# Kernel tuning notes

Measured on AMD Instinct MI355X. Metric: run time of the kernel, lower is better.

## Reference

```python
import jax, jax.numpy as jnp
import numpy as np

B, N, DIM = 2, 1024, 512
HEADS, DIM_HEAD = 8, 64
HIDDEN = HEADS * DIM_HEAD
TIME_DIM = 512
BIAS_DIM = 16
EPS = 1e-5


def setup_inputs() -> dict:
    key = jax.random.key(0)
    ks = jax.random.split(key, 12)
    inp = {
        "x": jax.random.normal(ks[0], (B, N, DIM), jnp.float32),
        "residx": jnp.broadcast_to(jnp.arange(N, dtype=jnp.float32), (B, N)),
        "time": jax.random.normal(ks[1], (B, 1, TIME_DIM), jnp.float32),
        "attn_bias": jax.random.normal(ks[2], (B, BIAS_DIM, N, N), jnp.float32),
        "seq_mask": jnp.ones((B, N), jnp.float32),
        # params
        "gamma": jnp.ones((DIM,), jnp.float32),
        "Wt": jax.random.normal(ks[3], (2 * DIM, TIME_DIM), jnp.float32) * 0.02,
        "bt": jax.random.normal(ks[4], (2 * DIM,), jnp.float32) * 0.02,
        "Wb": jax.random.normal(ks[5], (HEADS, BIAS_DIM), jnp.float32) * 0.1,
        "bb": jax.random.normal(ks[6], (HEADS,), jnp.float32) * 0.1,
        "Wq": jax.random.normal(ks[7], (HIDDEN, DIM), jnp.float32) * (DIM ** -0.5),
        "Wkv": jax.random.normal(ks[8], (2 * HIDDEN, DIM), jnp.float32) * (DIM ** -0.5),
        "Wo": jax.random.normal(ks[9], (DIM, HIDDEN), jnp.float32) * (HIDDEN ** -0.5),
    }
    return inp


def _layer_norm(x, gamma):
    mu = jnp.mean(x, axis=-1, keepdims=True)
    var = jnp.var(x, axis=-1, keepdims=True)
    return (x - mu) * jax.lax.rsqrt(var + EPS) * gamma  # beta buffer is zeros


def reference(x, residx, time, attn_bias, seq_mask, gamma, Wt, bt, Wb, bb, Wq, Wkv, Wo):
    h, d = HEADS, DIM_HEAD
    b, n, _ = x.shape
    xn = _layer_norm(x, gamma)
    # time conditioning: SiLU -> Linear -> chunk into scale/shift
    t = jax.nn.silu(time) @ Wt.T + bt  # [B,1,2*dim]
    scale, shift = jnp.split(t, 2, axis=-1)
    xn = xn * (scale + 1.0) + shift
    xn = xn * seq_mask[..., None]
    # projections
    q = (xn @ Wq.T).reshape(b, n, h, d).transpose(0, 2, 1, 3)  # b h n d
    kv = xn @ Wkv.T
    k_, v_ = jnp.split(kv, 2, axis=-1)
    k = k_.reshape(b, n, h, d).transpose(0, 2, 1, 3)
    v = v_.reshape(b, n, h, d).transpose(0, 2, 1, 3)
    q = q * (d ** -0.5)
    sim = jnp.einsum('bhid,bhjd->bhij', q, k)
    # attn bias projection: b a i j -> linear over a -> b h i j
    bias = jnp.einsum('baij,ha->bhij', attn_bias, Wb) + bb[None, :, None, None]
    sim = sim + bias
    # mask
    attn_mask = seq_mask[:, None, :, None] * seq_mask[:, None, None, :]  # b 1 i j
    sim = sim - (1.0 - attn_mask) * 1e6
    attn = jax.nn.softmax(sim, axis=-1)
    out = jnp.einsum('bhij,bhjd->bhid', attn, v)
    out = out.transpose(0, 2, 1, 3).reshape(b, n, h * d)
    out = out @ Wo.T
    out = out * seq_mask[..., None]
    return out
```

## Files before the change

### kernel.cpp

```cpp
#include <hip/hip_runtime.h>
#include <cstdint>
#include <cstddef>

typedef __bf16 bf16x8 __attribute__((ext_vector_type(8)));
typedef float f32x4 __attribute__((ext_vector_type(4)));
typedef unsigned int u32x4 __attribute__((ext_vector_type(4)));
typedef unsigned short u16;
typedef unsigned short u16x8 __attribute__((ext_vector_type(8)));

__device__ __forceinline__ u16 f2b(float f) {
    union { float f; uint32_t u; } v; v.f = f;
    uint32_t r = v.u + 0x7fffu + ((v.u >> 16) & 1u);
    return (u16)(r >> 16);
}
__device__ __forceinline__ float b2f(u16 h) {
    union { uint32_t u; float f; } v; v.u = ((uint32_t)h) << 16; return v.f;
}

__global__ __launch_bounds__(256) void prep_kernel(
    const float* __restrict__ Wq, const float* __restrict__ Wkv, const float* __restrict__ Wo,
    const float* __restrict__ timep, const float* __restrict__ Wt, const float* __restrict__ bt,
    u16* __restrict__ wqkv, u16* __restrict__ wo, float* __restrict__ tbuf)
{
    __shared__ float st[512];
    int bx = blockIdx.x, tid = threadIdx.x;
    if (bx < 1024) {
        int i = bx * 256 + tid;
        float4 v; u16* dp;
        if (i < 65536)      { v = ((const float4*)Wq)[i];            dp = wqkv + (size_t)i * 4; }
        else if (i < 196608){ int k = i - 65536;  v = ((const float4*)Wkv)[k]; dp = wqkv + 262144 + (size_t)k * 4; }
        else                { int k = i - 196608; v = ((const float4*)Wo)[k];  dp = wo + (size_t)k * 4; }
        ushort4 o;
        o.x = f2b(v.x); o.y = f2b(v.y); o.z = f2b(v.z); o.w = f2b(v.w);
        *(ushort4*)dp = o;
    } else {
        int bx2 = bx - 1024;
        int b = bx2 >> 2, ch = bx2 & 3;
        for (int k = tid; k < 512; k += 256) {
            float v = timep[b * 512 + k];
            st[k] = v / (1.f + __expf(-v));
        }
        __syncthreads();
        int o = ch * 256 + tid;
        const float4* wrow = (const float4*)(Wt + (size_t)o * 512);
        float acc = bt[o];
        #pragma unroll 4
        for (int k4 = 0; k4 < 128; k4++) {
            float4 w = wrow[k4];
            acc += st[k4*4+0]*w.x + st[k4*4+1]*w.y + st[k4*4+2]*w.z + st[k4*4+3]*w.w;
        }
        tbuf[b * 1024 + o] = acc;
    }
}

__global__ __launch_bounds__(64) void ln_cond_kernel(
    const float* __restrict__ x, const float* __restrict__ gamma,
    const float* __restrict__ tbuf, const float* __restrict__ seq_mask,
    u16* __restrict__ xn)
{
    int m = blockIdx.x;
    int b = m >> 10;
    int lane = threadIdx.x;
    const float* xr = x + (size_t)m * 512;
    int c0 = lane * 8;
    float4 v0 = *(const float4*)(xr + c0);
    float4 v1 = *(const float4*)(xr + c0 + 4);
    float xv[8] = {v0.x, v0.y, v0.z, v0.w, v1.x, v1.y, v1.z, v1.w};
    float s = 0.f, ss = 0.f;
    #pragma unroll
    for (int e = 0; e < 8; e++) { s += xv[e]; ss += xv[e]*xv[e]; }
    #pragma unroll
    for (int off = 1; off < 64; off <<= 1) {
        s  += __shfl_xor(s, off);
        ss += __shfl_xor(ss, off);
    }
    float mu = s * (1.f/512.f);
    float var = ss * (1.f/512.f) - mu*mu;
    float rs = rsqrtf(var + 1e-5f);
    float mk = seq_mask[m];
    u16x8 ov;
    #pragma unroll
    for (int e = 0; e < 8; e++) {
        int c = c0 + e;
        float sc = tbuf[b*1024 + c] + 1.f;
        float sh = tbuf[b*1024 + 512 + c];
        float val = ((xv[e] - mu) * rs * gamma[c] * sc + sh) * mk;
        ov[e] = f2b(val);
    }
    *(u16x8*)&xn[(size_t)m * 512 + c0] = ov;
}

__global__ __launch_bounds__(256) void bias_kernel(
    const float* __restrict__ ab, const float* __restrict__ Wb, const float* __restrict__ bbv,
    u16* __restrict__ bias_t)
{
    __shared__ u16 Ts[8 * 16 * 68];
    __shared__ float wbs[128];
    __shared__ float bbs[8];
    const int tid = threadIdx.x, bx = blockIdx.x;
    if (tid < 128) wbs[tid] = Wb[tid];
    if (tid < 8) bbs[tid] = bbv[tid];
    __syncthreads();
    int b = bx >> 10;
    int rem = bx & 1023;
    int i16 = rem >> 4, jt = rem & 15;
    int il = tid >> 4, jq = tid & 15;
    int i = i16*16 + il, j = jt*64 + jq*4;
    const float* p = ab + ((size_t)b << 24) + ((size_t)i << 10) + j;

#define LD(n) f32x4 v##n = __builtin_nontemporal_load((const f32x4*)(p + ((size_t)(n) << 20)));
    LD(0) LD(1) LD(2) LD(3) LD(4) LD(5) LD(6) LD(7)
    LD(8) LD(9) LD(10) LD(11) LD(12) LD(13) LD(14) LD(15)
#undef LD
#define FMAS(h) \
    f32x4 a##h = {bbs[h], bbs[h], bbs[h], bbs[h]}; \
    a##h += wbs[(h)*16+ 0]*v0;  a##h += wbs[(h)*16+ 1]*v1;  \
    a##h += wbs[(h)*16+ 2]*v2;  a##h += wbs[(h)*16+ 3]*v3;  \
    a##h += wbs[(h)*16+ 4]*v4;  a##h += wbs[(h)*16+ 5]*v5;  \
    a##h += wbs[(h)*16+ 6]*v6;  a##h += wbs[(h)*16+ 7]*v7;  \
    a##h += wbs[(h)*16+ 8]*v8;  a##h += wbs[(h)*16+ 9]*v9;  \
    a##h += wbs[(h)*16+10]*v10; a##h += wbs[(h)*16+11]*v11; \
    a##h += wbs[(h)*16+12]*v12; a##h += wbs[(h)*16+13]*v13; \
    a##h += wbs[(h)*16+14]*v14; a##h += wbs[(h)*16+15]*v15;
    FMAS(0) FMAS(1) FMAS(2) FMAS(3) FMAS(4) FMAS(5) FMAS(6) FMAS(7)
#undef FMAS
#define STT(h) { ushort4 o; \
    o.x = f2b(a##h[0]); o.y = f2b(a##h[1]); o.z = f2b(a##h[2]); o.w = f2b(a##h[3]); \
    *(ushort4*)&Ts[((h)*16 + il)*68 + jq*4] = o; }
    STT(0) STT(1) STT(2) STT(3) STT(4) STT(5) STT(6) STT(7)
#undef STT
    __syncthreads();
    int hh = tid >> 5, s0 = tid & 31;
    size_t tilebase = ((((size_t)(b*8 + hh))*32 + (i16 >> 1))*16 + jt)*2048 + (size_t)(i16 & 1)*1024;
    #pragma unroll
    for (int ss = 0; ss < 2; ss++) {
        int slot = s0 + ss*32;
        int g = slot >> 4, li = slot & 15;
        const u16* tb = &Ts[(hh*16 + g*4)*68 + li];
        unsigned w0 = (unsigned)tb[0*68+ 0] | ((unsigned)tb[0*68+16] << 16);
        unsigned w1 = (unsigned)tb[0*68+32] | ((unsigned)tb[0*68+48] << 16);
        unsigned w2 = (unsigned)tb[1*68+ 0] | ((unsigned)tb[1*68+16] << 16);
        unsigned w3 = (unsigned)tb[1*68+32] | ((unsigned)tb[1*68+48] << 16);
        unsigned w4 = (unsigned)tb[2*68+ 0] | ((unsigned)tb[2*68+16] << 16);
        unsigned w5 = (unsigned)tb[2*68+32] | ((unsigned)tb[2*68+48] << 16);
        unsigned w6 = (unsigned)tb[3*68+ 0] | ((unsigned)tb[3*68+16] << 16);
        unsigned w7 = (unsigned)tb[3*68+32] | ((unsigned)tb[3*68+48] << 16);
        u32x4 lo = {w0, w1, w2, w3};
        u32x4 hi = {w4, w5, w6, w7};
        __builtin_nontemporal_store(lo, (u32x4*)(bias_t + tilebase + (size_t)slot*16));
        __builtin_nontemporal_store(hi, (u32x4*)(bias_t + tilebase + (size_t)slot*16 + 8));
    }
}

__global__ __launch_bounds__(256) void qkv_gemm_kernel(
    const u16* __restrict__ xn, const u16* __restrict__ wqkv,
    u16* __restrict__ qb, u16* __restrict__ kb, u16* __restrict__ vT)
{
    __shared__ u16 As[128][40];
    __shared__ u16 Bs[128][40];
    const int tid = threadIdx.x;
    const int lane = tid & 63, wid = tid >> 6;
    const int wr = wid >> 1, wc = wid & 1;
    const int li = lane & 15, g = lane >> 4;
    const int m0 = blockIdx.x * 128, n0 = blockIdx.y * 128;

    f32x4 acc[4][4] = {};
    const int srow = tid >> 2, scol = (tid & 3) * 8;
    for (int k0 = 0; k0 < 512; k0 += 32) {
        *(bf16x8*)&As[srow][scol]      = *(const bf16x8*)&xn[(size_t)(m0+srow)*512 + k0 + scol];
        *(bf16x8*)&As[srow+64][scol]   = *(const bf16x8*)&xn[(size_t)(m0+srow+64)*512 + k0 + scol];
        *(bf16x8*)&Bs[srow][scol]      = *(const bf16x8*)&wqkv[(size_t)(n0+srow)*512 + k0 + scol];
        *(bf16x8*)&Bs[srow+64][scol]   = *(const bf16x8*)&wqkv[(size_t)(n0+srow+64)*512 + k0 + scol];
        __syncthreads();
        bf16x8 a[4], bf[4];
        #pragma unroll
        for (int mi = 0; mi < 4; mi++) a[mi]  = *(const bf16x8*)&As[wr*64 + mi*16 + li][g*8];
        #pragma unroll
        for (int nj = 0; nj < 4; nj++) bf[nj] = *(const bf16x8*)&Bs[wc*64 + nj*16 + li][g*8];
        #pragma unroll
        for (int mi = 0; mi < 4; mi++)
            #pragma unroll
            for (int nj = 0; nj < 4; nj++)
                acc[mi][nj] = __builtin_amdgcn_mfma_f32_16x16x32_bf16(a[mi], bf[nj], acc[mi][nj], 0, 0, 0);
        __syncthreads();
    }
    #pragma unroll
    for (int mi = 0; mi < 4; mi++)
        #pragma unroll
        for (int nj = 0; nj < 4; nj++) {
            int o = n0 + wc*64 + nj*16 + li;
            int m_base = m0 + wr*64 + mi*16 + g*4;
            if (o < 1024) {
                #pragma unroll
                for (int r = 0; r < 4; r++) {
                    int m = m_base + r;
                    int b = m >> 10, n = m & 1023;
                    float vv = acc[mi][nj][r];
                    if (o < 512) {
                        qb[((size_t)(b*8 + (o>>6))*1024 + n)*64 + (o&63)] = f2b(vv * 0.125f);
                    } else {
                        int oo = o - 512;
                        kb[((size_t)(b*8 + (oo>>6))*1024 + n)*64 + (oo&63)] = f2b(vv);
                    }
                }
            } else {
                int oo = o - 1024;
                int b = m_base >> 10, n = m_base & 1023;
                ushort4 ov;
                ov.x = f2b(acc[mi][nj][0]); ov.y = f2b(acc[mi][nj][1]);
                ov.z = f2b(acc[mi][nj][2]); ov.w = f2b(acc[mi][nj][3]);
                *(ushort4*)&vT[((size_t)(b*8 + (oo>>6))*64 + (oo&63))*1024 + n] = ov;
            }
        }
}

__global__ __launch_bounds__(256) void attn_kernel(
    const u16* __restrict__ qb, const u16* __restrict__ kb, const u16* __restrict__ vT,
    const u16* __restrict__ bias_t, const float* __restrict__ seq_mask,
    float* __restrict__ Om, float* __restrict__ ml)
{
    __shared__ u16 Ks[2][4096];
    __shared__ u16 Vs[2][4096];
    __shared__ u16 Ps[4][1024];
    __shared__ float mjs[512];
    int tid = threadIdx.x;
    int lane = tid & 63, w = tid >> 6;
    int li = lane & 15, g = lane >> 4;
    int it = blockIdx.x, h = blockIdx.y;
    int bz = blockIdx.z;
    int b = bz >> 1, jh = bz & 1;
    int bh = b*8 + h;
    int i0 = it * 64;
    int jt0 = jh * 8;
    const u16* qp = qb + ((size_t)bh*1024 + i0) * 64;
    const u16* kp = kb + (size_t)bh*65536 + (size_t)jt0*4096;
    const u16* vp = vT + (size_t)bh*65536;
    const u16* bp = bias_t + (((size_t)(bh*32 + it*2 + (w>>1)))*16 + jt0)*2048 + ((w&1)*64 + lane)*16;

    if (tid < 128) ((float4*)mjs)[tid] = ((const float4*)(seq_mask + b*1024 + jh*512))[tid];

    bf16x8 aq0 = *(const bf16x8*)&qp[(w*16 + li)*64 + g*8];
    bf16x8 aq1 = *(const bf16x8*)&qp[(w*16 + li)*64 + 32 + g*8];

    const int sli = tid & 15, sg = (tid >> 4) & 3, sf = tid >> 6;
    const int kslot0 = (sf*128 + sg*16 + sli) * 8;
    bf16x8 kr0, kr1, vr0, vr1, bfA_c, bfB_c, bfA_n, bfB_n;
    #define LOADT(jx) do { \
        kr0 = *(const bf16x8*)&kp[(size_t)(jx)*4096 + (sf*16 + sli)*64 + sg*8]; \
        kr1 = *(const bf16x8*)&kp[(size_t)(jx)*4096 + (sf*16 + sli)*64 + 32 + sg*8]; \
        vr0 = *(const bf16x8*)&vp[(size_t)(sf*16 + sli)*1024 + (jt0+(jx))*64 + sg*8]; \
        vr1 = *(const bf16x8*)&vp[(size_t)(sf*16 + sli)*1024 + (jt0+(jx))*64 + 32 + sg*8]; \
        bfA_n = *(const bf16x8*)&bp[(size_t)(jx)*2048]; \
        bfB_n = *(const bf16x8*)&bp[(size_t)(jx)*2048 + 8]; \
    } while (0)
    #define STORET(buf_) do { \
        *(bf16x8*)&Ks[buf_][kslot0]       = kr0; \
        *(bf16x8*)&Ks[buf_][kslot0 + 512] = kr1; \
        *(bf16x8*)&Vs[buf_][kslot0]       = vr0; \
        *(bf16x8*)&Vs[buf_][kslot0 + 512] = vr1; \
    } while (0)

    f32x4 oacc[4] = {};
    float m_run[4], l_run[4], mi[4];
    #pragma unroll
    for (int r = 0; r < 4; r++) {
        m_run[r] = -3e38f; l_run[r] = 0.f;
        mi[r] = seq_mask[b*1024 + i0 + w*16 + g*4 + r];
    }

    LOADT(0); STORET(0); bfA_c = bfA_n; bfB_c = bfB_n;
    __syncthreads();

    for (int jtt = 0; jtt < 8; jtt++) {
        int cur = jtt & 1;
        if (jtt < 7) LOADT(jtt + 1);
        f32x4 s[4] = {};
        #pragma unroll
        for (int fj = 0; fj < 4; fj++) {
            bf16x8 bk0 = *(const bf16x8*)&Ks[cur][(fj*128 + g*16 + li)*8];
            bf16x8 bk1 = *(const bf16x8*)&Ks[cur][(fj*128 + g*16 + li)*8 + 512];
            s[fj] = __builtin_amdgcn_mfma_f32_16x16x32_bf16(aq0, bk0, s[fj], 0, 0, 0);
            s[fj] = __builtin_amdgcn_mfma_f32_16x16x32_bf16(aq1, bk1, s[fj], 0, 0, 0);
        }
        float pmax[4] = {-3e38f, -3e38f, -3e38f, -3e38f};
        #pragma unroll
        for (int fj = 0; fj < 4; fj++) {
            float mj = mjs[jtt*64 + fj*16 + li];
            #pragma unroll
            for (int r = 0; r < 4; r++) {
                float bvl = (r < 2) ? b2f(((u16x8)bfA_c)[r*4 + fj]) : b2f(((u16x8)bfB_c)[(r-2)*4 + fj]);
                float sv = s[fj][r] + bvl;
                sv -= (1.f - mi[r]*mj) * 1e6f;
                s[fj][r] = sv;
                pmax[r] = fmaxf(pmax[r], sv);
            }
        }
        #pragma unroll
        for (int r = 0; r < 4; r++)
            #pragma unroll
            for (int off = 1; off < 16; off <<= 1)
                pmax[r] = fmaxf(pmax[r], __shfl_xor(pmax[r], off));
        float alpha[4], psum[4] = {0.f, 0.f, 0.f, 0.f}, mnew[4];
        #pragma unroll
        for (int r = 0; r < 4; r++) {
            mnew[r] = fmaxf(m_run[r], pmax[r]);
            alpha[r] = __expf(m_run[r] - mnew[r]);
            m_run[r] = mnew[r];
        }
        #pragma unroll
        for (int fj = 0; fj < 4; fj++)
            #pragma unroll
            for (int r = 0; r < 4; r++) {
                float p = __expf(s[fj][r] - mnew[r]);
                s[fj][r] = p;
                psum[r] += p;
            }
        #pragma unroll
        for (int r = 0; r < 4; r++) {
            #pragma unroll
            for (int off = 1; off < 16; off <<= 1) psum[r] += __shfl_xor(psum[r], off);
            l_run[r] = l_run[r]*alpha[r] + psum[r];
        }
        #pragma unroll
        for (int fj = 0; fj < 4; fj++) {
            int ph2 = fj >> 1;
            int pg = (fj*2 + (li >> 3)) & 3;
            int pin = li & 7;
            #pragma unroll
            for (int r = 0; r < 4; r++)
                Ps[w][(ph2*64 + pg*16 + g*4 + r)*8 + pin] = f2b(s[fj][r]);
        }
        #pragma unroll
        for (int fd = 0; fd < 4; fd++)
            #pragma unroll
            for (int r = 0; r < 4; r++)
                oacc[fd][r] *= alpha[r];
        bf16x8 ap0 = *(const bf16x8*)&Ps[w][(g*16 + li)*8];
        bf16x8 ap1 = *(const bf16x8*)&Ps[w][(g*16 + li)*8 + 512];
        #pragma unroll
        for (int fd = 0; fd < 4; fd++) {
            bf16x8 bv0 = *(const bf16x8*)&Vs[cur][(fd*128 + g*16 + li)*8];
            bf16x8 bv1 = *(const bf16x8*)&Vs[cur][(fd*128 + g*16 + li)*8 + 512];
            oacc[fd] = __builtin_amdgcn_mfma_f32_16x16x32_bf16(ap0, bv0, oacc[fd], 0, 0, 0);
            oacc[fd] = __builtin_amdgcn_mfma_f32_16x16x32_bf16(ap1, bv1, oacc[fd], 0, 0, 0);
        }
        if (jtt < 7) { STORET(cur ^ 1); bfA_c = bfA_n; bfB_c = bfB_n; }
        __syncthreads();
    }
    size_t pbase = ((size_t)(bh*16 + it)*2 + jh) * 4096;
    #pragma unroll
    for (int fd = 0; fd < 4; fd++)
        #pragma unroll
        for (int r = 0; r < 4; r++)
            Om[pbase + (size_t)(w*16 + g*4 + r)*64 + fd*16 + li] = oacc[fd][r];
    if (li == 0) {
        #pragma unroll
        for (int r = 0; r < 4; r++) {
            size_t mb = ((size_t)(bh*16 + it)*2 + jh) * 128 + (w*16 + g*4 + r)*2;
            ml[mb] = m_run[r]; ml[mb + 1] = l_run[r];
        }
    }
    #undef LOADT
    #undef STORET
}

__global__ __launch_bounds__(256) void merge_kernel(
    const float* __restrict__ Om, const float* __restrict__ ml, u16* __restrict__ aout)
{
    int blk = blockIdx.x;
    int bh = blk >> 4, it = blk & 15;
    int b = bh >> 3, h = bh & 7;
    int tid = threadIdx.x;
    int row = tid >> 2, dc = (tid & 3) * 16;
    size_t p0 = ((size_t)blk*2 + 0)*4096 + (size_t)row*64 + dc;
    size_t p1 = ((size_t)blk*2 + 1)*4096 + (size_t)row*64 + dc;
    size_t m0i = ((size_t)blk*2 + 0)*128 + row*2;
    size_t m1i = ((size_t)blk*2 + 1)*128 + row*2;
    float m0 = ml[m0i], l0 = ml[m0i + 1];
    float m1 = ml[m1i], l1 = ml[m1i + 1];
    float mm = fmaxf(m0, m1);
    float e0 = __expf(m0 - mm), e1 = __expf(m1 - mm);
    float linv = 1.f / (l0*e0 + l1*e1);
    int i = it*64 + row;
    u16* op = &aout[((size_t)(b*1024 + i))*512 + h*64 + dc];
    #pragma unroll
    for (int c4 = 0; c4 < 4; c4++) {
        f32x4 v0 = *(const f32x4*)&Om[p0 + c4*4];
        f32x4 v1 = *(const f32x4*)&Om[p1 + c4*4];
        ushort4 o;
        o.x = f2b((v0[0]*e0 + v1[0]*e1)*linv);
        o.y = f2b((v0[1]*e0 + v1[1]*e1)*linv);
        o.z = f2b((v0[2]*e0 + v1[2]*e1)*linv);
        o.w = f2b((v0[3]*e0 + v1[3]*e1)*linv);
        *(ushort4*)&op[c4*4] = o;
    }
}

__global__ __launch_bounds__(256) void out_gemm_kernel(
    const u16* __restrict__ aout, const u16* __restrict__ wo,
    const float* __restrict__ seq_mask, float* __restrict__ out)
{
    __shared__ u16 As[64][40];
    __shared__ u16 Bs[64][40];
    const int tid = threadIdx.x;
    const int lane = tid & 63, wid = tid >> 6;
    const int wr = wid >> 1, wc = wid & 1;
    const int li = lane & 15, g = lane >> 4;
    const int m0 = blockIdx.x * 64, n0 = blockIdx.y * 64;

    f32x4 acc[2][2] = {};
    const int lrow = tid >> 2, lcol = (tid & 3) * 8;
    for (int k0 = 0; k0 < 512; k0 += 32) {
        *(bf16x8*)&As[lrow][lcol] = *(const bf16x8*)&aout[(size_t)(m0+lrow)*512 + k0 + lcol];
        *(bf16x8*)&Bs[lrow][lcol] = *(const bf16x8*)&wo[(size_t)(n0+lrow)*512 + k0 + lcol];
        __syncthreads();
        bf16x8 a[2], bf[2];
        #pragma unroll
        for (int fi = 0; fi < 2; fi++) a[fi]  = *(const bf16x8*)&As[wr*32 + fi*16 + li][g*8];
        #pragma unroll
        for (int fj = 0; fj < 2; fj++) bf[fj] = *(const bf16x8*)&Bs[wc*32 + fj*16 + li][g*8];
        #pragma unroll
        for (int fi = 0; fi < 2; fi++)
            #pragma unroll
            for (int fj = 0; fj < 2; fj++)
                acc[fi][fj] = __builtin_amdgcn_mfma_f32_16x16x32_bf16(a[fi], bf[fj], acc[fi][fj], 0, 0, 0);
        __syncthreads();
    }
    #pragma unroll
    for (int fi = 0; fi < 2; fi++)
        #pragma unroll
        for (int fj = 0; fj < 2; fj++)
            #pragma unroll
            for (int r = 0; r < 4; r++) {
                int m = m0 + wr*32 + fi*16 + g*4 + r;
                int o = n0 + wc*32 + fj*16 + li;
                out[(size_t)m*512 + o] = acc[fi][fj][r] * seq_mask[m];
            }
}

extern "C" void kernel_launch(void* const* d_in, const int* in_sizes, int n_in,
                              void* d_out, int out_size, void* d_ws, size_t ws_size,
                              hipStream_t stream) {
    const float* x         = (const float*)d_in[0];
    const float* timep     = (const float*)d_in[2];
    const float* attn_bias = (const float*)d_in[3];
    const float* seq_mask  = (const float*)d_in[4];
    const float* gamma     = (const float*)d_in[5];
    const float* Wt        = (const float*)d_in[6];
    const float* bt        = (const float*)d_in[7];
    const float* Wb        = (const float*)d_in[8];
    const float* bb        = (const float*)d_in[9];
    const float* Wq        = (const float*)d_in[10];
    const float* Wkv       = (const float*)d_in[11];
    const float* Wo        = (const float*)d_in[12];
    float* out = (float*)d_out;

    char* ws = (char*)d_ws;
    size_t off = 0;
    auto alloc = [&](size_t bytes) { char* p = ws + off; off += (bytes + 255) & ~(size_t)255; return p; };
    float* tbuf  = (float*)alloc(2 * 1024 * 4);
    u16* xn      = (u16*)alloc((size_t)2048 * 512 * 2);
    u16* wqkv    = (u16*)alloc((size_t)1536 * 512 * 2);
    u16* wo      = (u16*)alloc((size_t)512 * 512 * 2);
    u16* qb      = (u16*)alloc((size_t)2 * 8 * 1024 * 64 * 2);
    u16* kb      = (u16*)alloc((size_t)2 * 8 * 1024 * 64 * 2);
    u16* vT      = (u16*)alloc((size_t)2 * 8 * 64 * 1024 * 2);
    u16* bias_t  = (u16*)alloc((size_t)2 * 8 * 1024 * 1024 * 2);
    u16* aout    = (u16*)alloc((size_t)2048 * 512 * 2);
    float* Om    = (float*)alloc((size_t)256 * 2 * 4096 * 4);
    float* ml    = (float*)alloc((size_t)256 * 2 * 128 * 4);
    (void)ws_size;

    bias_kernel<<<2048, 256, 0, stream>>>(attn_bias, Wb, bb, bias_t);
    prep_kernel<<<1032, 256, 0, stream>>>(Wq, Wkv, Wo, timep, Wt, bt, wqkv, wo, tbuf);
    ln_cond_kernel<<<2048, 64, 0, stream>>>(x, gamma, tbuf, seq_mask, xn);
    qkv_gemm_kernel<<<dim3(16, 12), 256, 0, stream>>>(xn, wqkv, qb, kb, vT);
    attn_kernel<<<dim3(16, 8, 4), 256, 0, stream>>>(qb, kb, vT, bias_t, seq_mask, Om, ml);
    merge_kernel<<<256, 256, 0, stream>>>(Om, ml, aout);
    out_gemm_kernel<<<dim3(32, 8), 256, 0, stream>>>(aout, wo, seq_mask, out);
}
```

Baseline: 106.8 us.

## Merge attn-bias projection and QKV GEMM into one heterogeneous launch

The separate bias projection kernel and QKV GEMM kernel become a single launch. The first 192 blocks run the GEMM and the remaining 2048 blocks run the bias projection. The bias blocks are also retiled so each block covers 4 rows by 256 columns instead of 16 rows by 64 columns, with a new shared-memory transpose layout. The aim is to remove a launch and let the memory-bound bias work overlap with the compute-bound GEMM, at the cost of a shared LDS footprint sized for the larger of the two roles.

```diff
diff --git a/kernel.cpp b/kernel.cpp
--- a/kernel.cpp
+++ b/kernel.cpp
@@ -90,128 +90,138 @@
     *(u16x8*)&xn[(size_t)m * 512 + c0] = ov;
 }
 
-__global__ __launch_bounds__(256) void bias_kernel(
+__global__ __launch_bounds__(256) void qkv_bias_kernel(
     const float* __restrict__ ab, const float* __restrict__ Wb, const float* __restrict__ bbv,
-    u16* __restrict__ bias_t)
-{
-    __shared__ u16 Ts[8 * 16 * 68];
+    const u16* __restrict__ xn, const u16* __restrict__ wqkv,
+    u16* __restrict__ bias_t, u16* __restrict__ qb, u16* __restrict__ kb, u16* __restrict__ vT)
+{
+    __shared__ u16 SH[10240];
     __shared__ float wbs[128];
     __shared__ float bbs[8];
-    const int tid = threadIdx.x, bx = blockIdx.x;
-    if (tid < 128) wbs[tid] = Wb[tid];
-    if (tid < 8) bbs[tid] = bbv[tid];
-    __syncthreads();
-    int b = bx >> 10;
-    int rem = bx & 1023;
-    int i16 = rem >> 4, jt = rem & 15;
-    int il = tid >> 4, jq = tid & 15;
-    int i = i16*16 + il, j = jt*64 + jq*4;
-    const float* p = ab + ((size_t)b << 24) + ((size_t)i << 10) + j;
+    const int tid = threadIdx.x;
+    const int bx = blockIdx.x;
+    if (bx >= 192) {
+        if (tid < 128) wbs[tid] = Wb[tid];
+        if (tid < 8) bbs[tid] = bbv[tid];
+        __syncthreads();
+        int bx2 = bx - 192;
+        int b = bx2 >> 10;
+        int rem = bx2 & 1023;
+        int i4 = rem >> 2, jq = rem & 3;
+        int w = tid >> 6, lane = tid & 63;
+        int i = i4*4 + w;
+        int col = jq*256 + lane*4;
+        const float* p = ab + ((size_t)b << 24) + ((size_t)i << 10) + col;
 
 #define LD(n) f32x4 v##n = __builtin_nontemporal_load((const f32x4*)(p + ((size_t)(n) << 20)));
-    LD(0) LD(1) LD(2) LD(3) LD(4) LD(5) LD(6) LD(7)
-    LD(8) LD(9) LD(10) LD(11) LD(12) LD(13) LD(14) LD(15)
+        LD(0) LD(1) LD(2) LD(3) LD(4) LD(5) LD(6) LD(7)
+        LD(8) LD(9) LD(10) LD(11) LD(12) LD(13) LD(14) LD(15)
 #undef LD
 #define FMAS(h) \
-    f32x4 a##h = {bbs[h], bbs[h], bbs[h], bbs[h]}; \
-    a##h += wbs[(h)*16+ 0]*v0;  a##h += wbs[(h)*16+ 1]*v1;  \
-    a##h += wbs[(h)*16+ 2]*v2;  a##h += wbs[(h)*16+ 3]*v3;  \
-    a##h += wbs[(h)*16+ 4]*v4;  a##h += wbs[(h)*16+ 5]*v5;  \
-    a##h += wbs[(h)*16+ 6]*v6;  a##h += wbs[(h)*16+ 7]*v7;  \
-    a##h += wbs[(h)*16+ 8]*v8;  a##h += wbs[(h)*16+ 9]*v9;  \
-    a##h += wbs[(h)*16+10]*v10; a##h += wbs[(h)*16+11]*v11; \
-    a##h += wbs[(h)*16+12]*v12; a##h += wbs[(h)*16+13]*v13; \
-    a##h += wbs[(h)*16+14]*v14; a##h += wbs[(h)*16+15]*v15;
-    FMAS(0) FMAS(1) FMAS(2) FMAS(3) FMAS(4) FMAS(5) FMAS(6) FMAS(7)
+        f32x4 a##h = {bbs[h], bbs[h], bbs[h], bbs[h]}; \
+        a##h += wbs[(h)*16+ 0]*v0;  a##h += wbs[(h)*16+ 1]*v1;  \
+        a##h += wbs[(h)*16+ 2]*v2;  a##h += wbs[(h)*16+ 3]*v3;  \
+        a##h += wbs[(h)*16+ 4]*v4;  a##h += wbs[(h)*16+ 5]*v5;  \
+        a##h += wbs[(h)*16+ 6]*v6;  a##h += wbs[(h)*16+ 7]*v7;  \
+        a##h += wbs[(h)*16+ 8]*v8;  a##h += wbs[(h)*16+ 9]*v9;  \
+        a##h += wbs[(h)*16+10]*v10; a##h += wbs[(h)*16+11]*v11; \
+        a##h += wbs[(h)*16+12]*v12; a##h += wbs[(h)*16+13]*v13; \
+        a##h += wbs[(h)*16+14]*v14; a##h += wbs[(h)*16+15]*v15;
+        FMAS(0) FMAS(1) FMAS(2) FMAS(3) FMAS(4) FMAS(5) FMAS(6) FMAS(7)
 #undef FMAS
+        {
+            int jt_l = lane >> 4, wc = (lane & 15) * 4;
 #define STT(h) { ushort4 o; \
-    o.x = f2b(a##h[0]); o.y = f2b(a##h[1]); o.z = f2b(a##h[2]); o.w = f2b(a##h[3]); \
-    *(ushort4*)&Ts[((h)*16 + il)*68 + jq*4] = o; }
-    STT(0) STT(1) STT(2) STT(3) STT(4) STT(5) STT(6) STT(7)
+            o.x = f2b(a##h[0]); o.y = f2b(a##h[1]); o.z = f2b(a##h[2]); o.w = f2b(a##h[3]); \
+            *(ushort4*)&SH[((h)*4 + w)*280 + jt_l*68 + wc] = o; }
+            STT(0) STT(1) STT(2) STT(3) STT(4) STT(5) STT(6) STT(7)
 #undef STT
-    __syncthreads();
-    int hh = tid >> 5, s0 = tid & 31;
-    size_t tilebase = ((((size_t)(b*8 + hh))*32 + (i16 >> 1))*16 + jt)*2048 + (size_t)(i16 & 1)*1024;
-    #pragma unroll
-    for (int ss = 0; ss < 2; ss++) {
-        int slot = s0 + ss*32;
-        int g = slot >> 4, li = slot & 15;
-        const u16* tb = &Ts[(hh*16 + g*4)*68 + li];
-        unsigned w0 = (unsigned)tb[0*68+ 0] | ((unsigned)tb[0*68+16] << 16);
-        unsigned w1 = (unsigned)tb[0*68+32] | ((unsigned)tb[0*68+48] << 16);
-        unsigned w2 = (unsigned)tb[1*68+ 0] | ((unsigned)tb[1*68+16] << 16);
-        unsigned w3 = (unsigned)tb[1*68+32] | ((unsigned)tb[1*68+48] << 16);
-        unsigned w4 = (unsigned)tb[2*68+ 0] | ((unsigned)tb[2*68+16] << 16);
-        unsigned w5 = (unsigned)tb[2*68+32] | ((unsigned)tb[2*68+48] << 16);
-        unsigned w6 = (unsigned)tb[3*68+ 0] | ((unsigned)tb[3*68+16] << 16);
-        unsigned w7 = (unsigned)tb[3*68+32] | ((unsigned)tb[3*68+48] << 16);
-        u32x4 lo = {w0, w1, w2, w3};
-        u32x4 hi = {w4, w5, w6, w7};
-        __builtin_nontemporal_store(lo, (u32x4*)(bias_t + tilebase + (size_t)slot*16));
-        __builtin_nontemporal_store(hi, (u32x4*)(bias_t + tilebase + (size_t)slot*16 + 8));
-    }
-}
-
-__global__ __launch_bounds__(256) void qkv_gemm_kernel(
-    const u16* __restrict__ xn, const u16* __restrict__ wqkv,
-    u16* __restrict__ qb, u16* __restrict__ kb, u16* __restrict__ vT)
-{
-    __shared__ u16 As[128][40];
-    __shared__ u16 Bs[128][40];
-    const int tid = threadIdx.x;
-    const int lane = tid & 63, wid = tid >> 6;
-    const int wr = wid >> 1, wc = wid & 1;
-    const int li = lane & 15, g = lane >> 4;
-    const int m0 = blockIdx.x * 128, n0 = blockIdx.y * 128;
-
-    f32x4 acc[4][4] = {};
-    const int srow = tid >> 2, scol = (tid & 3) * 8;
-    for (int k0 = 0; k0 < 512; k0 += 32) {
-        *(bf16x8*)&As[srow][scol]      = *(const bf16x8*)&xn[(size_t)(m0+srow)*512 + k0 + scol];
-        *(bf16x8*)&As[srow+64][scol]   = *(const bf16x8*)&xn[(size_t)(m0+srow+64)*512 + k0 + scol];
-        *(bf16x8*)&Bs[srow][scol]      = *(const bf16x8*)&wqkv[(size_t)(n0+srow)*512 + k0 + scol];
-        *(bf16x8*)&Bs[srow+64][scol]   = *(const bf16x8*)&wqkv[(size_t)(n0+srow+64)*512 + k0 + scol];
-        __syncthreads();
-        bf16x8 a[4], bf[4];
-        #pragma unroll
-        for (int mi = 0; mi < 4; mi++) a[mi]  = *(const bf16x8*)&As[wr*64 + mi*16 + li][g*8];
-        #pragma unroll
-        for (int nj = 0; nj < 4; nj++) bf[nj] = *(const bf16x8*)&Bs[wc*64 + nj*16 + li][g*8];
+        }
+        __syncthreads();
+        int hh = tid >> 5, s0 = tid & 31;
+        int it32 = i4 >> 3, isub = (i4 >> 2) & 1, g = i4 & 3;
+        #pragma unroll
+        for (int ss = 0; ss < 2; ss++) {
+            int sl = s0 + ss*32;
+            int jt_l = sl >> 4, li = sl & 15;
+            int jt = jq*4 + jt_l;
+            const u16* tb = &SH[(hh*4)*280 + jt_l*68 + li];
+            u16 t0  = tb[0*280 +  0], t1  = tb[0*280 + 16], t2  = tb[0*280 + 32], t3  = tb[0*280 + 48];
+            u16 t4  = tb[1*280 +  0], t5  = tb[1*280 + 16], t6  = tb[1*280 + 32], t7  = tb[1*280 + 48];
+            u16 t8  = tb[2*280 +  0], t9  = tb[2*280 + 16], t10 = tb[2*280 + 32], t11 = tb[2*280 + 48];
+            u16 t12 = tb[3*280 +  0], t13 = tb[3*280 + 16], t14 = tb[3*280 + 32], t15 = tb[3*280 + 48];
+            unsigned w0 = (unsigned)t0  | ((unsigned)t1  << 16);
+            unsigned w1 = (unsigned)t2  | ((unsigned)t3  << 16);
+            unsigned w2 = (unsigned)t4  | ((unsigned)t5  << 16);
+            unsigned w3 = (unsigned)t6  | ((unsigned)t7  << 16);
+            unsigned w4 = (unsigned)t8  | ((unsigned)t9  << 16);
+            unsigned w5 = (unsigned)t10 | ((unsigned)t11 << 16);
+            unsigned w6 = (unsigned)t12 | ((unsigned)t13 << 16);
+            unsigned w7 = (unsigned)t14 | ((unsigned)t15 << 16);
+            int slot = isub*64 + g*16 + li;
+            size_t tbse = ((((size_t)(b*8 + hh))*32 + it32)*16 + jt)*2048 + (size_t)slot*16;
+            u32x4 lo = {w0, w1, w2, w3};
+            u32x4 hi = {w4, w5, w6, w7};
+            __builtin_nontemporal_store(lo, (u32x4*)(bias_t + tbse));
+            __builtin_nontemporal_store(hi, (u32x4*)(bias_t + tbse + 8));
+        }
+    } else {
+        u16 (*As)[40] = (u16(*)[40])&SH[0];
+        u16 (*Bs)[40] = (u16(*)[40])&SH[5120];
+        int v = bx;
+        const int m0 = (v & 15) * 128, n0 = (v >> 4) * 128;
+        const int lane = tid & 63, wid = tid >> 6;
+        const int wr = wid >> 1, wc = wid & 1;
+        const int li = lane & 15, g = lane >> 4;
+        f32x4 acc[4][4] = {};
+        const int srow = tid >> 2, scol = (tid & 3) * 8;
+        for (int k0 = 0; k0 < 512; k0 += 32) {
+            *(bf16x8*)&As[srow][scol]      = *(const bf16x8*)&xn[(size_t)(m0+srow)*512 + k0 + scol];
+            *(bf16x8*)&As[srow+64][scol]   = *(const bf16x8*)&xn[(size_t)(m0+srow+64)*512 + k0 + scol];
+            *(bf16x8*)&Bs[srow][scol]      = *(const bf16x8*)&wqkv[(size_t)(n0+srow)*512 + k0 + scol];
+            *(bf16x8*)&Bs[srow+64][scol]   = *(const bf16x8*)&wqkv[(size_t)(n0+srow+64)*512 + k0 + scol];
+            __syncthreads();
+            bf16x8 a[4], bf[4];
+            #pragma unroll
+            for (int mi = 0; mi < 4; mi++) a[mi]  = *(const bf16x8*)&As[wr*64 + mi*16 + li][g*8];
+            #pragma unroll
+            for (int nj = 0; nj < 4; nj++) bf[nj] = *(const bf16x8*)&Bs[wc*64 + nj*16 + li][g*8];
+            #pragma unroll
+            for (int mi = 0; mi < 4; mi++)
+                #pragma unroll
+                for (int nj = 0; nj < 4; nj++)
+                    acc[mi][nj] = __builtin_amdgcn_mfma_f32_16x16x32_bf16(a[mi], bf[nj], acc[mi][nj], 0, 0, 0);
+            __syncthreads();
+        }
         #pragma unroll
         for (int mi = 0; mi < 4; mi++)
             #pragma unroll
-            for (int nj = 0; nj < 4; nj++)
-                acc[mi][nj] = __builtin_amdgcn_mfma_f32_16x16x32_bf16(a[mi], bf[nj], acc[mi][nj], 0, 0, 0);
-        __syncthreads();
-    }
-    #pragma unroll
-    for (int mi = 0; mi < 4; mi++)
-        #pragma unroll
-        for (int nj = 0; nj < 4; nj++) {
-            int o = n0 + wc*64 + nj*16 + li;
-            int m_base = m0 + wr*64 + mi*16 + g*4;
-            if (o < 1024) {
-                #pragma unroll
-                for (int r = 0; r < 4; r++) {
-                    int m = m_base + r;
-                    int b = m >> 10, n = m & 1023;
-                    float vv = acc[mi][nj][r];
-                    if (o < 512) {
-                        qb[((size_t)(b*8 + (o>>6))*1024 + n)*64 + (o&63)] = f2b(vv * 0.125f);
-                    } else {
-                        int oo = o - 512;
-                        kb[((size_t)(b*8 + (oo>>6))*1024 + n)*64 + (oo&63)] = f2b(vv);
+            for (int nj = 0; nj < 4; nj++) {
+                int o = n0 + wc*64 + nj*16 + li;
+                int m_base = m0 + wr*64 + mi*16 + g*4;
+                if (o < 1024) {
+                    #pragma unroll
+                    for (int r = 0; r < 4; r++) {
+                        int m = m_base + r;
+                        int b = m >> 10, n = m & 1023;
+                        float vv = acc[mi][nj][r];
+                        if (o < 512) {
+                            qb[((size_t)(b*8 + (o>>6))*1024 + n)*64 + (o&63)] = f2b(vv * 0.125f);
+                        } else {
+                            int oo = o - 512;
+                            kb[((size_t)(b*8 + (oo>>6))*1024 + n)*64 + (oo&63)] = f2b(vv);
+                        }
                     }
+                } else {
+                    int oo = o - 1024;
+                    int b = m_base >> 10, n = m_base & 1023;
+                    ushort4 ov;
+                    ov.x = f2b(acc[mi][nj][0]); ov.y = f2b(acc[mi][nj][1]);
+                    ov.z = f2b(acc[mi][nj][2]); ov.w = f2b(acc[mi][nj][3]);
+                    *(ushort4*)&vT[((size_t)(b*8 + (oo>>6))*64 + (oo&63))*1024 + n] = ov;
                 }
-            } else {
-                int oo = o - 1024;
-                int b = m_base >> 10, n = m_base & 1023;
-                ushort4 ov;
-                ov.x = f2b(acc[mi][nj][0]); ov.y = f2b(acc[mi][nj][1]);
-                ov.z = f2b(acc[mi][nj][2]); ov.w = f2b(acc[mi][nj][3]);
-                *(ushort4*)&vT[((size_t)(b*8 + (oo>>6))*64 + (oo&63))*1024 + n] = ov;
             }
-        }
+    }
 }
 
 __global__ __launch_bounds__(256) void attn_kernel(
@@ -471,10 +481,9 @@
     float* ml    = (float*)alloc((size_t)256 * 2 * 128 * 4);
     (void)ws_size;
 
-    bias_kernel<<<2048, 256, 0, stream>>>(attn_bias, Wb, bb, bias_t);
     prep_kernel<<<1032, 256, 0, stream>>>(Wq, Wkv, Wo, timep, Wt, bt, wqkv, wo, tbuf);
     ln_cond_kernel<<<2048, 64, 0, stream>>>(x, gamma, tbuf, seq_mask, xn);
-    qkv_gemm_kernel<<<dim3(16, 12), 256, 0, stream>>>(xn, wqkv, qb, kb, vT);
+    qkv_bias_kernel<<<2240, 256, 0, stream>>>(attn_bias, Wb, bb, xn, wqkv, bias_t, qb, kb, vT);
     attn_kernel<<<dim3(16, 8, 4), 256, 0, stream>>>(qb, kb, vT, bias_t, seq_mask, Om, ml);
     merge_kernel<<<256, 256, 0, stream>>>(Om, ml, aout);
     out_gemm_kernel<<<dim3(32, 8), 256, 0, stream>>>(aout, wo, seq_mask, out);
```

Result: faster. 96.21 us (-9.9%).

## Fuse bias projection into QKV GEMM launch and drop attention split-K merge

Applied to the files above, without the earlier changes.

The bias projection and QKV GEMM now share one launch: the first 192 blocks run the GEMM tiles and the rest do the bias projection into the shared LDS buffer. This lets the GEMM overlap with the memory-bound bias pass. The attention kernel no longer splits the key range in two. Each block covers all 16 key tiles and writes normalized bf16 output directly, which removes the fp32 partial buffers and the merge kernel. The cost is half as many attention blocks (256 instead of 512), so occupancy drops and each block runs a longer serial loop. The bias loads are also split into two passes of eight to lower register pressure.

```diff
diff --git a/kernel.cpp b/kernel.cpp
--- a/kernel.cpp
+++ b/kernel.cpp
@@ -90,154 +90,156 @@
     *(u16x8*)&xn[(size_t)m * 512 + c0] = ov;
 }
 
-__global__ __launch_bounds__(256) void bias_kernel(
+__global__ __launch_bounds__(256) void qkv_bias_kernel(
     const float* __restrict__ ab, const float* __restrict__ Wb, const float* __restrict__ bbv,
-    u16* __restrict__ bias_t)
+    const u16* __restrict__ xn, const u16* __restrict__ wqkv,
+    u16* __restrict__ bias_t, u16* __restrict__ qb, u16* __restrict__ kb, u16* __restrict__ vT)
 {
-    __shared__ u16 Ts[8 * 16 * 68];
+    __shared__ u16 SH[10240];
     __shared__ float wbs[128];
     __shared__ float bbs[8];
-    const int tid = threadIdx.x, bx = blockIdx.x;
-    if (tid < 128) wbs[tid] = Wb[tid];
-    if (tid < 8) bbs[tid] = bbv[tid];
-    __syncthreads();
-    int b = bx >> 10;
-    int rem = bx & 1023;
-    int i16 = rem >> 4, jt = rem & 15;
-    int il = tid >> 4, jq = tid & 15;
-    int i = i16*16 + il, j = jt*64 + jq*4;
-    const float* p = ab + ((size_t)b << 24) + ((size_t)i << 10) + j;
-
-#define LD(n) f32x4 v##n = __builtin_nontemporal_load((const f32x4*)(p + ((size_t)(n) << 20)));
-    LD(0) LD(1) LD(2) LD(3) LD(4) LD(5) LD(6) LD(7)
-    LD(8) LD(9) LD(10) LD(11) LD(12) LD(13) LD(14) LD(15)
+    const int tid = threadIdx.x;
+    const int bx = blockIdx.x;
+    if (bx >= 192) {
+        if (tid < 128) wbs[tid] = Wb[tid];
+        if (tid < 8) bbs[tid] = bbv[tid];
+        __syncthreads();
+        int bx2 = bx - 192;
+        int b = bx2 >> 10;
+        int rem = bx2 & 1023;
+        int i16 = rem >> 4, jt = rem & 15;
+        int il = tid >> 4, jq = tid & 15;
+        int i = i16*16 + il, j = jt*64 + jq*4;
+        const float* p = ab + ((size_t)b << 24) + ((size_t)i << 10) + j;
+
+        f32x4 a0 = {bbs[0], bbs[0], bbs[0], bbs[0]};
+        f32x4 a1 = {bbs[1], bbs[1], bbs[1], bbs[1]};
+        f32x4 a2 = {bbs[2], bbs[2], bbs[2], bbs[2]};
+        f32x4 a3 = {bbs[3], bbs[3], bbs[3], bbs[3]};
+        f32x4 a4 = {bbs[4], bbs[4], bbs[4], bbs[4]};
+        f32x4 a5 = {bbs[5], bbs[5], bbs[5], bbs[5]};
+        f32x4 a6 = {bbs[6], bbs[6], bbs[6], bbs[6]};
+        f32x4 a7 = {bbs[7], bbs[7], bbs[7], bbs[7]};
+        #pragma unroll
+        for (int pass = 0; pass < 2; pass++) {
+            int a8 = pass * 8;
+#define LD(n) f32x4 v##n = __builtin_nontemporal_load((const f32x4*)(p + ((size_t)(a8 + n) << 20)));
+            LD(0) LD(1) LD(2) LD(3) LD(4) LD(5) LD(6) LD(7)
 #undef LD
 #define FMAS(h) \
-    f32x4 a##h = {bbs[h], bbs[h], bbs[h], bbs[h]}; \
-    a##h += wbs[(h)*16+ 0]*v0;  a##h += wbs[(h)*16+ 1]*v1;  \
-    a##h += wbs[(h)*16+ 2]*v2;  a##h += wbs[(h)*16+ 3]*v3;  \
-    a##h += wbs[(h)*16+ 4]*v4;  a##h += wbs[(h)*16+ 5]*v5;  \
-    a##h += wbs[(h)*16+ 6]*v6;  a##h += wbs[(h)*16+ 7]*v7;  \
-    a##h += wbs[(h)*16+ 8]*v8;  a##h += wbs[(h)*16+ 9]*v9;  \
-    a##h += wbs[(h)*16+10]*v10; a##h += wbs[(h)*16+11]*v11; \
-    a##h += wbs[(h)*16+12]*v12; a##h += wbs[(h)*16+13]*v13; \
-    a##h += wbs[(h)*16+14]*v14; a##h += wbs[(h)*16+15]*v15;
-    FMAS(0) FMAS(1) FMAS(2) FMAS(3) FMAS(4) FMAS(5) FMAS(6) FMAS(7)
+            a##h += wbs[(h)*16 + a8 + 0]*v0; a##h += wbs[(h)*16 + a8 + 1]*v1; \
+            a##h += wbs[(h)*16 + a8 + 2]*v2; a##h += wbs[(h)*16 + a8 + 3]*v3; \
+            a##h += wbs[(h)*16 + a8 + 4]*v4; a##h += wbs[(h)*16 + a8 + 5]*v5; \
+            a##h += wbs[(h)*16 + a8 + 6]*v6; a##h += wbs[(h)*16 + a8 + 7]*v7;
+            FMAS(0) FMAS(1) FMAS(2) FMAS(3) FMAS(4) FMAS(5) FMAS(6) FMAS(7)
 #undef FMAS
+        }
 #define STT(h) { ushort4 o; \
-    o.x = f2b(a##h[0]); o.y = f2b(a##h[1]); o.z = f2b(a##h[2]); o.w = f2b(a##h[3]); \
-    *(ushort4*)&Ts[((h)*16 + il)*68 + jq*4] = o; }
-    STT(0) STT(1) STT(2) STT(3) STT(4) STT(5) STT(6) STT(7)
+        o.x = f2b(a##h[0]); o.y = f2b(a##h[1]); o.z = f2b(a##h[2]); o.w = f2b(a##h[3]); \
+        *(ushort4*)&SH[((h)*16 + il)*68 + jq*4] = o; }
+        STT(0) STT(1) STT(2) STT(3) STT(4) STT(5) STT(6) STT(7)
 #undef STT
-    __syncthreads();
-    int hh = tid >> 5, s0 = tid & 31;
-    size_t tilebase = ((((size_t)(b*8 + hh))*32 + (i16 >> 1))*16 + jt)*2048 + (size_t)(i16 & 1)*1024;
-    #pragma unroll
-    for (int ss = 0; ss < 2; ss++) {
-        int slot = s0 + ss*32;
-        int g = slot >> 4, li = slot & 15;
-        const u16* tb = &Ts[(hh*16 + g*4)*68 + li];
-        unsigned w0 = (unsigned)tb[0*68+ 0] | ((unsigned)tb[0*68+16] << 16);
-        unsigned w1 = (unsigned)tb[0*68+32] | ((unsigned)tb[0*68+48] << 16);
-        unsigned w2 = (unsigned)tb[1*68+ 0] | ((unsigned)tb[1*68+16] << 16);
-        unsigned w3 = (unsigned)tb[1*68+32] | ((unsigned)tb[1*68+48] << 16);
-        unsigned w4 = (unsigned)tb[2*68+ 0] | ((unsigned)tb[2*68+16] << 16);
-        unsigned w5 = (unsigned)tb[2*68+32] | ((unsigned)tb[2*68+48] << 16);
-        unsigned w6 = (unsigned)tb[3*68+ 0] | ((unsigned)tb[3*68+16] << 16);
-        unsigned w7 = (unsigned)tb[3*68+32] | ((unsigned)tb[3*68+48] << 16);
-        u32x4 lo = {w0, w1, w2, w3};
-        u32x4 hi = {w4, w5, w6, w7};
-        __builtin_nontemporal_store(lo, (u32x4*)(bias_t + tilebase + (size_t)slot*16));
-        __builtin_nontemporal_store(hi, (u32x4*)(bias_t + tilebase + (size_t)slot*16 + 8));
-    }
-}
-
-__global__ __launch_bounds__(256) void qkv_gemm_kernel(
-    const u16* __restrict__ xn, const u16* __restrict__ wqkv,
-    u16* __restrict__ qb, u16* __restrict__ kb, u16* __restrict__ vT)
-{
-    __shared__ u16 As[128][40];
-    __shared__ u16 Bs[128][40];
-    const int tid = threadIdx.x;
-    const int lane = tid & 63, wid = tid >> 6;
-    const int wr = wid >> 1, wc = wid & 1;
-    const int li = lane & 15, g = lane >> 4;
-    const int m0 = blockIdx.x * 128, n0 = blockIdx.y * 128;
-
-    f32x4 acc[4][4] = {};
-    const int srow = tid >> 2, scol = (tid & 3) * 8;
-    for (int k0 = 0; k0 < 512; k0 += 32) {
-        *(bf16x8*)&As[srow][scol]      = *(const bf16x8*)&xn[(size_t)(m0+srow)*512 + k0 + scol];
-        *(bf16x8*)&As[srow+64][scol]   = *(const bf16x8*)&xn[(size_t)(m0+srow+64)*512 + k0 + scol];
-        *(bf16x8*)&Bs[srow][scol]      = *(const bf16x8*)&wqkv[(size_t)(n0+srow)*512 + k0 + scol];
-        *(bf16x8*)&Bs[srow+64][scol]   = *(const bf16x8*)&wqkv[(size_t)(n0+srow+64)*512 + k0 + scol];
-        __syncthreads();
-        bf16x8 a[4], bf[4];
-        #pragma unroll
-        for (int mi = 0; mi < 4; mi++) a[mi]  = *(const bf16x8*)&As[wr*64 + mi*16 + li][g*8];
-        #pragma unroll
-        for (int nj = 0; nj < 4; nj++) bf[nj] = *(const bf16x8*)&Bs[wc*64 + nj*16 + li][g*8];
+        __syncthreads();
+        int hh = tid >> 5, s0 = tid & 31;
+        size_t tilebase = ((((size_t)(b*8 + hh))*32 + (i16 >> 1))*16 + jt)*2048 + (size_t)(i16 & 1)*1024;
+        #pragma unroll
+        for (int ss = 0; ss < 2; ss++) {
+            int slot = s0 + ss*32;
+            int g = slot >> 4, li = slot & 15;
+            const u16* tb = &SH[(hh*16 + g*4)*68 + li];
+            unsigned w0 = (unsigned)tb[0*68+ 0] | ((unsigned)tb[0*68+16] << 16);
+            unsigned w1 = (unsigned)tb[0*68+32] | ((unsigned)tb[0*68+48] << 16);
+            unsigned w2 = (unsigned)tb[1*68+ 0] | ((unsigned)tb[1*68+16] << 16);
+            unsigned w3 = (unsigned)tb[1*68+32] | ((unsigned)tb[1*68+48] << 16);
+            unsigned w4 = (unsigned)tb[2*68+ 0] | ((unsigned)tb[2*68+16] << 16);
+            unsigned w5 = (unsigned)tb[2*68+32] | ((unsigned)tb[2*68+48] << 16);
+            unsigned w6 = (unsigned)tb[3*68+ 0] | ((unsigned)tb[3*68+16] << 16);
+            unsigned w7 = (unsigned)tb[3*68+32] | ((unsigned)tb[3*68+48] << 16);
+            u32x4 lo = {w0, w1, w2, w3};
+            u32x4 hi = {w4, w5, w6, w7};
+            __builtin_nontemporal_store(lo, (u32x4*)(bias_t + tilebase + (size_t)slot*16));
+            __builtin_nontemporal_store(hi, (u32x4*)(bias_t + tilebase + (size_t)slot*16 + 8));
+        }
+    } else {
+        u16 (*As)[40] = (u16(*)[40])&SH[0];
+        u16 (*Bs)[40] = (u16(*)[40])&SH[5120];
+        int v = bx;
+        const int m0 = (v & 15) * 128, n0 = (v >> 4) * 128;
+        const int lane = tid & 63, wid = tid >> 6;
+        const int wr = wid >> 1, wc = wid & 1;
+        const int li = lane & 15, g = lane >> 4;
+        f32x4 acc[4][4] = {};
+        const int srow = tid >> 2, scol = (tid & 3) * 8;
+        for (int k0 = 0; k0 < 512; k0 += 32) {
+            *(bf16x8*)&As[srow][scol]      = *(const bf16x8*)&xn[(size_t)(m0+srow)*512 + k0 + scol];
+            *(bf16x8*)&As[srow+64][scol]   = *(const bf16x8*)&xn[(size_t)(m0+srow+64)*512 + k0 + scol];
+            *(bf16x8*)&Bs[srow][scol]      = *(const bf16x8*)&wqkv[(size_t)(n0+srow)*512 + k0 + scol];
+            *(bf16x8*)&Bs[srow+64][scol]   = *(const bf16x8*)&wqkv[(size_t)(n0+srow+64)*512 + k0 + scol];
+            __syncthreads();
+            bf16x8 a[4], bf[4];
+            #pragma unroll
+            for (int mi = 0; mi < 4; mi++) a[mi]  = *(const bf16x8*)&As[wr*64 + mi*16 + li][g*8];
+            #pragma unroll
+            for (int nj = 0; nj < 4; nj++) bf[nj] = *(const bf16x8*)&Bs[wc*64 + nj*16 + li][g*8];
+            #pragma unroll
+            for (int mi = 0; mi < 4; mi++)
+                #pragma unroll
+                for (int nj = 0; nj < 4; nj++)
+                    acc[mi][nj] = __builtin_amdgcn_mfma_f32_16x16x32_bf16(a[mi], bf[nj], acc[mi][nj], 0, 0, 0);
+            __syncthreads();
+        }
         #pragma unroll
         for (int mi = 0; mi < 4; mi++)
             #pragma unroll
-            for (int nj = 0; nj < 4; nj++)
-                acc[mi][nj] = __builtin_amdgcn_mfma_f32_16x16x32_bf16(a[mi], bf[nj], acc[mi][nj], 0, 0, 0);
-        __syncthreads();
-    }
-    #pragma unroll
-    for (int mi = 0; mi < 4; mi++)
-        #pragma unroll
-        for (int nj = 0; nj < 4; nj++) {
-            int o = n0 + wc*64 + nj*16 + li;
-            int m_base = m0 + wr*64 + mi*16 + g*4;
-            if (o < 1024) {
-                #pragma unroll
-                for (int r = 0; r < 4; r++) {
-                    int m = m_base + r;
-                    int b = m >> 10, n = m & 1023;
-                    float vv = acc[mi][nj][r];
-                    if (o < 512) {
-                        qb[((size_t)(b*8 + (o>>6))*1024 + n)*64 + (o&63)] = f2b(vv * 0.125f);
-                    } else {
-                        int oo = o - 512;
-                        kb[((size_t)(b*8 + (oo>>6))*1024 + n)*64 + (oo&63)] = f2b(vv);
+            for (int nj = 0; nj < 4; nj++) {
+                int o = n0 + wc*64 + nj*16 + li;
+                int m_base = m0 + wr*64 + mi*16 + g*4;
+                if (o < 1024) {
+                    #pragma unroll
+                    for (int r = 0; r < 4; r++) {
+                        int m = m_base + r;
+                        int b = m >> 10, n = m & 1023;
+                        float vv = acc[mi][nj][r];
+                        if (o < 512) {
+                            qb[((size_t)(b*8 + (o>>6))*1024 + n)*64 + (o&63)] = f2b(vv * 0.125f);
+                        } else {
+                            int oo = o - 512;
+                            kb[((size_t)(b*8 + (oo>>6))*1024 + n)*64 + (oo&63)] = f2b(vv);
+                        }
                     }
+                } else {
+                    int oo = o - 1024;
+                    int b = m_base >> 10, n = m_base & 1023;
+                    ushort4 ov;
+                    ov.x = f2b(acc[mi][nj][0]); ov.y = f2b(acc[mi][nj][1]);
+                    ov.z = f2b(acc[mi][nj][2]); ov.w = f2b(acc[mi][nj][3]);
+                    *(ushort4*)&vT[((size_t)(b*8 + (oo>>6))*64 + (oo&63))*1024 + n] = ov;
                 }
-            } else {
-                int oo = o - 1024;
-                int b = m_base >> 10, n = m_base & 1023;
-                ushort4 ov;
-                ov.x = f2b(acc[mi][nj][0]); ov.y = f2b(acc[mi][nj][1]);
-                ov.z = f2b(acc[mi][nj][2]); ov.w = f2b(acc[mi][nj][3]);
-                *(ushort4*)&vT[((size_t)(b*8 + (oo>>6))*64 + (oo&63))*1024 + n] = ov;
             }
-        }
+    }
 }
 
 __global__ __launch_bounds__(256) void attn_kernel(
     const u16* __restrict__ qb, const u16* __restrict__ kb, const u16* __restrict__ vT,
     const u16* __restrict__ bias_t, const float* __restrict__ seq_mask,
-    float* __restrict__ Om, float* __restrict__ ml)
+    u16* __restrict__ aout)
 {
     __shared__ u16 Ks[2][4096];
     __shared__ u16 Vs[2][4096];
     __shared__ u16 Ps[4][1024];
-    __shared__ float mjs[512];
+    __shared__ float mjs[1024];
     int tid = threadIdx.x;
     int lane = tid & 63, w = tid >> 6;
     int li = lane & 15, g = lane >> 4;
-    int it = blockIdx.x, h = blockIdx.y;
-    int bz = blockIdx.z;
-    int b = bz >> 1, jh = bz & 1;
+    int it = blockIdx.x, h = blockIdx.y, b = blockIdx.z;
     int bh = b*8 + h;
     int i0 = it * 64;
-    int jt0 = jh * 8;
     const u16* qp = qb + ((size_t)bh*1024 + i0) * 64;
-    const u16* kp = kb + (size_t)bh*65536 + (size_t)jt0*4096;
+    const u16* kp = kb + (size_t)bh*65536;
     const u16* vp = vT + (size_t)bh*65536;
-    const u16* bp = bias_t + (((size_t)(bh*32 + it*2 + (w>>1)))*16 + jt0)*2048 + ((w&1)*64 + lane)*16;
-
-    if (tid < 128) ((float4*)mjs)[tid] = ((const float4*)(seq_mask + b*1024 + jh*512))[tid];
+    const u16* bp = bias_t + (((size_t)(bh*32 + it*2 + (w>>1)))*16)*2048 + ((w&1)*64 + lane)*16;
+
+    ((float4*)mjs)[tid] = ((const float4*)(seq_mask + b*1024))[tid];
 
     bf16x8 aq0 = *(const bf16x8*)&qp[(w*16 + li)*64 + g*8];
     bf16x8 aq1 = *(const bf16x8*)&qp[(w*16 + li)*64 + 32 + g*8];
@@ -248,8 +250,8 @@
     #define LOADT(jx) do { \
         kr0 = *(const bf16x8*)&kp[(size_t)(jx)*4096 + (sf*16 + sli)*64 + sg*8]; \
         kr1 = *(const bf16x8*)&kp[(size_t)(jx)*4096 + (sf*16 + sli)*64 + 32 + sg*8]; \
-        vr0 = *(const bf16x8*)&vp[(size_t)(sf*16 + sli)*1024 + (jt0+(jx))*64 + sg*8]; \
-        vr1 = *(const bf16x8*)&vp[(size_t)(sf*16 + sli)*1024 + (jt0+(jx))*64 + 32 + sg*8]; \
+        vr0 = *(const bf16x8*)&vp[(size_t)(sf*16 + sli)*1024 + (jx)*64 + sg*8]; \
+        vr1 = *(const bf16x8*)&vp[(size_t)(sf*16 + sli)*1024 + (jx)*64 + 32 + sg*8]; \
         bfA_n = *(const bf16x8*)&bp[(size_t)(jx)*2048]; \
         bfB_n = *(const bf16x8*)&bp[(size_t)(jx)*2048 + 8]; \
     } while (0)
@@ -271,9 +273,9 @@
     LOADT(0); STORET(0); bfA_c = bfA_n; bfB_c = bfB_n;
     __syncthreads();
 
-    for (int jtt = 0; jtt < 8; jtt++) {
+    for (int jtt = 0; jtt < 16; jtt++) {
         int cur = jtt & 1;
-        if (jtt < 7) LOADT(jtt + 1);
+        if (jtt < 15) LOADT(jtt + 1);
         f32x4 s[4] = {};
         #pragma unroll
         for (int fj = 0; fj < 4; fj++) {
@@ -344,56 +346,19 @@
             oacc[fd] = __builtin_amdgcn_mfma_f32_16x16x32_bf16(ap0, bv0, oacc[fd], 0, 0, 0);
             oacc[fd] = __builtin_amdgcn_mfma_f32_16x16x32_bf16(ap1, bv1, oacc[fd], 0, 0, 0);
         }
-        if (jtt < 7) { STORET(cur ^ 1); bfA_c = bfA_n; bfB_c = bfB_n; }
-        __syncthreads();
-    }
-    size_t pbase = ((size_t)(bh*16 + it)*2 + jh) * 4096;
-    #pragma unroll
-    for (int fd = 0; fd < 4; fd++)
-        #pragma unroll
-        for (int r = 0; r < 4; r++)
-            Om[pbase + (size_t)(w*16 + g*4 + r)*64 + fd*16 + li] = oacc[fd][r];
-    if (li == 0) {
-        #pragma unroll
-        for (int r = 0; r < 4; r++) {
-            size_t mb = ((size_t)(bh*16 + it)*2 + jh) * 128 + (w*16 + g*4 + r)*2;
-            ml[mb] = m_run[r]; ml[mb + 1] = l_run[r];
-        }
+        if (jtt < 15) { STORET(cur ^ 1); bfA_c = bfA_n; bfB_c = bfB_n; }
+        __syncthreads();
+    }
+    #pragma unroll
+    for (int r = 0; r < 4; r++) {
+        int i = i0 + w*16 + g*4 + r;
+        float linv = 1.f / l_run[r];
+        #pragma unroll
+        for (int fd = 0; fd < 4; fd++)
+            aout[((size_t)(b*1024 + i))*512 + h*64 + fd*16 + li] = f2b(oacc[fd][r] * linv);
     }
     #undef LOADT
     #undef STORET
-}
-
-__global__ __launch_bounds__(256) void merge_kernel(
-    const float* __restrict__ Om, const float* __restrict__ ml, u16* __restrict__ aout)
-{
-    int blk = blockIdx.x;
-    int bh = blk >> 4, it = blk & 15;
-    int b = bh >> 3, h = bh & 7;
-    int tid = threadIdx.x;
-    int row = tid >> 2, dc = (tid & 3) * 16;
-    size_t p0 = ((size_t)blk*2 + 0)*4096 + (size_t)row*64 + dc;
-    size_t p1 = ((size_t)blk*2 + 1)*4096 + (size_t)row*64 + dc;
-    size_t m0i = ((size_t)blk*2 + 0)*128 + row*2;
-    size_t m1i = ((size_t)blk*2 + 1)*128 + row*2;
-    float m0 = ml[m0i], l0 = ml[m0i + 1];
-    float m1 = ml[m1i], l1 = ml[m1i + 1];
-    float mm = fmaxf(m0, m1);
-    float e0 = __expf(m0 - mm), e1 = __expf(m1 - mm);
-    float linv = 1.f / (l0*e0 + l1*e1);
-    int i = it*64 + row;
-    u16* op = &aout[((size_t)(b*1024 + i))*512 + h*64 + dc];
-    #pragma unroll
-    for (int c4 = 0; c4 < 4; c4++) {
-        f32x4 v0 = *(const f32x4*)&Om[p0 + c4*4];
-        f32x4 v1 = *(const f32x4*)&Om[p1 + c4*4];
-        ushort4 o;
-        o.x = f2b((v0[0]*e0 + v1[0]*e1)*linv);
-        o.y = f2b((v0[1]*e0 + v1[1]*e1)*linv);
-        o.z = f2b((v0[2]*e0 + v1[2]*e1)*linv);
-        o.w = f2b((v0[3]*e0 + v1[3]*e1)*linv);
-        *(ushort4*)&op[c4*4] = o;
-    }
 }
 
 __global__ __launch_bounds__(256) void out_gemm_kernel(
@@ -467,15 +432,11 @@
     u16* vT      = (u16*)alloc((size_t)2 * 8 * 64 * 1024 * 2);
     u16* bias_t  = (u16*)alloc((size_t)2 * 8 * 1024 * 1024 * 2);
     u16* aout    = (u16*)alloc((size_t)2048 * 512 * 2);
-    float* Om    = (float*)alloc((size_t)256 * 2 * 4096 * 4);
-    float* ml    = (float*)alloc((size_t)256 * 2 * 128 * 4);
     (void)ws_size;
 
-    bias_kernel<<<2048, 256, 0, stream>>>(attn_bias, Wb, bb, bias_t);
     prep_kernel<<<1032, 256, 0, stream>>>(Wq, Wkv, Wo, timep, Wt, bt, wqkv, wo, tbuf);
     ln_cond_kernel<<<2048, 64, 0, stream>>>(x, gamma, tbuf, seq_mask, xn);
-    qkv_gemm_kernel<<<dim3(16, 12), 256, 0, stream>>>(xn, wqkv, qb, kb, vT);
-    attn_kernel<<<dim3(16, 8, 4), 256, 0, stream>>>(qb, kb, vT, bias_t, seq_mask, Om, ml);
-    merge_kernel<<<256, 256, 0, stream>>>(Om, ml, aout);
+    qkv_bias_kernel<<<2240, 256, 0, stream>>>(attn_bias, Wb, bb, xn, wqkv, bias_t, qb, kb, vT);
+    attn_kernel<<<dim3(16, 8, 2), 256, 0, stream>>>(qb, kb, vT, bias_t, seq_mask, aout);
     out_gemm_kernel<<<dim3(32, 8), 256, 0, stream>>>(aout, wo, seq_mask, out);
 }
```

Result: faster. 98.02 us (-8.2%).
